# Optimization experiments

Hardware: AMD Instinct MI355X
Metric: run time of the kernel (lower is better)

## Reference

```python
import jax, jax.numpy as jnp
import numpy as np

B, N, D, H, DH, G = 4, 16384, 256, 8, 64, 64  # batch, tokens, dim, heads, dim_head, slice_num
INNER = H * DH

def _gelu(t):
    return jax.nn.gelu(t, approximate=False)  # torch nn.GELU default is exact erf

def setup_inputs() -> dict:
    key = jax.random.key(0)
    ks = jax.random.split(key, 12)
    s = lambda k, shape, sc: jax.random.normal(k, shape, jnp.float32) * sc
    return {
        "x": jax.random.normal(ks[0], (B, N, D), jnp.float32),
        "Wx": s(ks[1], (INNER, D), 0.05), "bx": jnp.zeros((INNER,), jnp.float32),
        "W1": s(ks[2], (G, DH), 0.1), "b1": jnp.zeros((G,), jnp.float32),
        "W2": s(ks[3], (1, G), 0.1), "b2": jnp.zeros((1,), jnp.float32),
        "bias": jnp.full((1, H, 1, 1), 0.5, jnp.float32),
        "Ws": s(ks[4], (G, DH), 0.1), "bs": jnp.zeros((G,), jnp.float32),
        "Wq": s(ks[5], (DH, DH), 0.1),
        "Wk": s(ks[6], (DH, DH), 0.1),
        "Wv": s(ks[7], (DH, DH), 0.1),
        "Wo": s(ks[8], (D, INNER), 0.05), "bo": jnp.zeros((D,), jnp.float32),
        "u": jax.random.uniform(ks[9], (B, H, N, G), jnp.float32),  # gumbel base noise
    }

def reference(x, Wx, bx, W1, b1, W2, b2, bias, Ws, bs, Wq, Wk, Wv, Wo, bo, u):
    b, n, d = x.shape
    h, dh = bias.shape[1], Wq.shape[0]
    # project and split heads: [B,H,N,dh]
    x_mid = (x @ Wx.T + bx).reshape(b, n, h, dh).transpose(0, 2, 1, 3)
    # per-token temperature MLP + learned bias, clamped
    temp = _gelu(_gelu(x_mid @ W1.T + b1) @ W2.T + b2) + bias  # [B,H,N,1]
    temp = jnp.clip(temp, 0.01)
    # gumbel-softmax soft slice routing
    logits = x_mid @ Ws.T + bs                                  # [B,H,N,G]
    gnoise = -jnp.log(-jnp.log(u + 1e-8) + 1e-8)
    slice_w = jax.nn.softmax((logits + gnoise) / temp, axis=-1)  # [B,H,N,G]
    # weighted pooling into slice tokens
    slice_norm = slice_w.sum(axis=2)                             # [B,H,G]
    slice_tok = jnp.einsum('bhnc,bhng->bhgc', x_mid, slice_w)
    slice_tok = slice_tok / (slice_norm + 1e-5)[..., None]       # [B,H,G,dh]
    # attention over the G slice tokens
    q = slice_tok @ Wq.T
    k = slice_tok @ Wk.T
    v = slice_tok @ Wv.T
    scale = 1.0 / np.sqrt(dh).astype(np.float32)
    attn = jax.nn.softmax(jnp.einsum('bhgc,bhkc->bhgk', q, k) * scale, axis=-1)
    out_s = jnp.einsum('bhgk,bhkc->bhgc', attn, v)               # [B,H,G,dh]
    # scatter back to tokens via slice weights
    out_x = jnp.einsum('bhgc,bhng->bhnc', out_s, slice_w)        # [B,H,N,dh]
    out_x = out_x.transpose(0, 2, 1, 3).reshape(b, n, h * dh)
    return out_x @ Wo.T + bo
```

## Files before the change

kernel.cpp:

```cpp
#include <hip/hip_runtime.h>

constexpr int B_ = 4;
constexpr int N_ = 16384;
constexpr int D_ = 256;
constexpr int H_ = 8;
constexpr int DH_ = 64;
constexpr int G_ = 64;
constexpr int INNER_ = 512;

typedef __attribute__((ext_vector_type(8))) short bf16x8;
typedef __attribute__((ext_vector_type(4))) float f32x4;

__device__ __forceinline__ unsigned short f2bu(float f) {
  union { float f; unsigned int u; } v; v.f = f;
  unsigned int r = v.u + 0x7FFFu + ((v.u >> 16) & 1u);
  return (unsigned short)(r >> 16);
}
__device__ __forceinline__ float bu2f(unsigned short h) {
  union { unsigned int u; float f; } v; v.u = ((unsigned int)h) << 16;
  return v.f;
}
__device__ __forceinline__ float gelu_f(float x) {
  const float ax = fabsf(x);
  const float y = ax * 0.70710678118654752440f;
  const float t = 1.0f / fmaf(0.3275911f, y, 1.0f);
  float poly = 1.061405429f;
  poly = fmaf(poly, t, -1.453152027f);
  poly = fmaf(poly, t, 1.421413741f);
  poly = fmaf(poly, t, -0.284496736f);
  poly = fmaf(poly, t, 0.254829592f);
  poly *= t;
  const float e = __expf(-y * y);
  const float E = fmaf(-poly, e, 1.0f);
  return fmaf(0.5f * ax, E, 0.5f * x);
}

__global__ __launch_bounds__(256) void cast_kernel(const float* __restrict__ in,
                                                   unsigned short* __restrict__ o, int n) {
  int i = (blockIdx.x * 256 + threadIdx.x) * 4;
  if (i + 3 < n) {
    float4 v = *reinterpret_cast<const float4*>(&in[i]);
    o[i + 0] = f2bu(v.x);
    o[i + 1] = f2bu(v.y);
    o[i + 2] = f2bu(v.z);
    o[i + 3] = f2bu(v.w);
  }
}

__global__ __launch_bounds__(256) void prep_wrb_kernel(const float* __restrict__ W1,
                                                       const float* __restrict__ Ws,
                                                       unsigned short* __restrict__ WrB) {
  const int i = blockIdx.x * 256 + threadIdx.x;
  if (i < 8192) {
    const int row = i >> 6, col = i & 63;
    const float v = (row < 64) ? W1[row * 64 + col] : Ws[(row - 64) * 64 + col];
    WrB[i] = f2bu(v);
  }
}

template <int MODE>
__global__ __launch_bounds__(256)
void gemm_bt_kernel(const float* __restrict__ Af32,
                    const unsigned short* __restrict__ Abf,
                    const unsigned short* __restrict__ Bt,
                    unsigned short* __restrict__ Cbf,
                    float* __restrict__ Cf32,
                    const float* __restrict__ bias) {
  constexpr int K = (MODE == 0) ? 256 : 512;
  __shared__ unsigned short As[128][72];
  __shared__ unsigned short Bs[128][72];

  const int tid = threadIdx.x;
  const int lane = tid & 63;
  const int wid = tid >> 6;
  const int wm = wid >> 1;
  const int wn = wid & 1;
  const long m0 = (long)blockIdx.x * 128;
  const int n0 = blockIdx.y * 128;

  long aBase = 0, btBase = 0, cBase = 0;
  if constexpr (MODE == 1) {
    const long z = blockIdx.z;
    aBase = z * (long)N_ * 512;
    btBase = z * (long)D_ * 512;
    cBase = z * (long)N_ * D_;
  }

  f32x4 acc[4][4];
#pragma unroll
  for (int m = 0; m < 4; ++m)
#pragma unroll
    for (int n = 0; n < 4; ++n) acc[m][n] = (f32x4){0.f, 0.f, 0.f, 0.f};

  for (int t = 0; t < K / 64; ++t) {
    const int k0 = t * 64;
    if constexpr (MODE == 0) {
#pragma unroll
      for (int i = 0; i < 8; ++i) {
        const int flat = i * 1024 + tid * 4;
        const int r = flat >> 6;
        const int kk = flat & 63;
        const float4 v = *reinterpret_cast<const float4*>(&Af32[(m0 + r) * 256 + k0 + kk]);
        unsigned short tmp[4] = {f2bu(v.x), f2bu(v.y), f2bu(v.z), f2bu(v.w)};
        *reinterpret_cast<unsigned long long*>(&As[r][kk]) =
            *reinterpret_cast<unsigned long long*>(tmp);
      }
    } else {
#pragma unroll
      for (int i = 0; i < 4; ++i) {
        const int flat = i * 2048 + tid * 8;
        const int r = flat >> 6;
        const int kk = flat & 63;
        *reinterpret_cast<int4*>(&As[r][kk]) =
            *reinterpret_cast<const int4*>(&Abf[aBase + (m0 + r) * (long)K + k0 + kk]);
      }
    }
#pragma unroll
    for (int i = 0; i < 4; ++i) {
      const int flat = i * 2048 + tid * 8;
      const int c = flat >> 6;
      const int kk = flat & 63;
      *reinterpret_cast<int4*>(&Bs[c][kk]) =
          *reinterpret_cast<const int4*>(&Bt[btBase + (n0 + c) * (long)K + k0 + kk]);
    }
    __syncthreads();
#pragma unroll
    for (int kk = 0; kk < 2; ++kk) {
      bf16x8 a[4], bb[4];
#pragma unroll
      for (int m = 0; m < 4; ++m)
        a[m] = *reinterpret_cast<const bf16x8*>(
            &As[wm * 64 + m * 16 + (lane & 15)][kk * 32 + (lane >> 4) * 8]);
#pragma unroll
      for (int n = 0; n < 4; ++n)
        bb[n] = *reinterpret_cast<const bf16x8*>(
            &Bs[wn * 64 + n * 16 + (lane & 15)][kk * 32 + (lane >> 4) * 8]);
#pragma unroll
      for (int m = 0; m < 4; ++m)
#pragma unroll
        for (int n = 0; n < 4; ++n)
          acc[m][n] = __builtin_amdgcn_mfma_f32_16x16x32_bf16(a[m], bb[n], acc[m][n], 0, 0, 0);
    }
    __syncthreads();
  }
#pragma unroll
  for (int n = 0; n < 4; ++n) {
    const int c = n0 + wn * 64 + n * 16 + (lane & 15);
    const float bv = bias[c];
#pragma unroll
    for (int m = 0; m < 4; ++m) {
      const long rb = m0 + wm * 64 + m * 16 + ((lane >> 4) << 2);
#pragma unroll
      for (int j = 0; j < 4; ++j) {
        const float val = acc[m][n][j] + bv;
        if constexpr (MODE == 0) {
          Cbf[(rb + j) * 512 + c] = f2bu(val);
        } else {
          Cf32[cBase + (rb + j) * 256 + c] = val;
        }
      }
    }
  }
}

__global__ __launch_bounds__(256)
void routing_fused_kernel(const unsigned short* __restrict__ xmid,
                          const unsigned short* __restrict__ WrB,
                          const float* __restrict__ u,
                          const float* __restrict__ b1,
                          const float* __restrict__ W2,
                          const float* __restrict__ b2,
                          const float* __restrict__ biasH,
                          const float* __restrict__ bs,
                          unsigned short* __restrict__ wout) {
  __shared__ union SM {
    struct { unsigned short As[64][72]; unsigned short Bs[128][72]; } s;
    float hl[64 * 67];
  } sm;
  __shared__ float cw2[64], cb1[64], cbs[64], cbh[8];
  __shared__ float tempL[64];

  const int tid = threadIdx.x;
  const int lane = tid & 63;
  const int wid = tid >> 6;
  const int wm = wid >> 1;
  const int wn = wid & 1;
  const int q = lane >> 4;
  const int c15 = lane & 15;

  if (tid < 64) {
    cw2[tid] = W2[tid];
    cb1[tid] = b1[tid];
    cbs[tid] = bs[tid];
  }
  if (tid < 8) cbh[tid] = biasH[tid];
  const float b2g = b2[0];

  const unsigned short* Ablk = xmid + (long)blockIdx.x * 4096;
#pragma unroll
  for (int i = 0; i < 2; ++i) {
    const int idx = i * 256 + tid;
    const int row = idx >> 3;
    const int col = (idx & 7) * 8;
    *reinterpret_cast<int4*>(&sm.s.As[row][col]) = *reinterpret_cast<const int4*>(Ablk + idx * 8);
  }
#pragma unroll
  for (int i = 0; i < 4; ++i) {
    const int idx = i * 256 + tid;
    const int row = idx >> 3;
    const int col = (idx & 7) * 8;
    *reinterpret_cast<int4*>(&sm.s.Bs[row][col]) = *reinterpret_cast<const int4*>(WrB + idx * 8);
  }
  __syncthreads();

  f32x4 acc[2][4];
#pragma unroll
  for (int m = 0; m < 2; ++m)
#pragma unroll
    for (int n = 0; n < 4; ++n) acc[m][n] = (f32x4){0.f, 0.f, 0.f, 0.f};

#pragma unroll
  for (int kk = 0; kk < 2; ++kk) {
    bf16x8 a[2], bb[4];
#pragma unroll
    for (int m = 0; m < 2; ++m)
      a[m] = *reinterpret_cast<const bf16x8*>(
          &sm.s.As[wm * 32 + m * 16 + c15][kk * 32 + q * 8]);
#pragma unroll
    for (int n = 0; n < 4; ++n)
      bb[n] = *reinterpret_cast<const bf16x8*>(
          &sm.s.Bs[wn * 64 + n * 16 + c15][kk * 32 + q * 8]);
#pragma unroll
    for (int m = 0; m < 2; ++m)
#pragma unroll
      for (int n = 0; n < 4; ++n)
        acc[m][n] = __builtin_amdgcn_mfma_f32_16x16x32_bf16(a[m], bb[n], acc[m][n], 0, 0, 0);
  }
  __syncthreads();

  if (wn == 0) {
    float b1v[4];
#pragma unroll
    for (int n = 0; n < 4; ++n) b1v[n] = cb1[n * 16 + c15];
#pragma unroll
    for (int m = 0; m < 2; ++m) {
      const int rb = wm * 32 + m * 16 + q * 4;
#pragma unroll
      for (int n = 0; n < 4; ++n) {
        const int c = n * 16 + c15;
#pragma unroll
        for (int j = 0; j < 4; ++j)
          sm.hl[(rb + j) * 67 + c] = acc[m][n][j] + b1v[n];
      }
    }
  }
  __syncthreads();

  const int r_e = tid >> 2;
  const int quarter = tid & 3;
  const int g0 = quarter * 16;
  const long t_e = (long)blockIdx.x * 64 + r_e;
  const int h_e = (int)(t_e & 7);

  float sdot = 0.f;
#pragma unroll
  for (int j = 0; j < 16; ++j)
    sdot = fmaf(gelu_f(sm.hl[r_e * 67 + g0 + j]), cw2[g0 + j], sdot);
  sdot += __shfl_xor(sdot, 1);
  sdot += __shfl_xor(sdot, 2);
  if (quarter == 0) {
    float temp = gelu_f(sdot + b2g) + cbh[h_e];
    temp = fmaxf(temp, 0.01f);
    tempL[r_e] = 1.0f / temp;
  }
  __syncthreads();

  if (wn == 1) {
    float bsv[4];
#pragma unroll
    for (int n = 0; n < 4; ++n) bsv[n] = cbs[n * 16 + c15];
#pragma unroll
    for (int m = 0; m < 2; ++m) {
      const int rb = wm * 32 + m * 16 + q * 4;
#pragma unroll
      for (int n = 0; n < 4; ++n) {
        const int c = n * 16 + c15;
#pragma unroll
        for (int j = 0; j < 4; ++j)
          sm.hl[(rb + j) * 67 + c] = acc[m][n][j] + bsv[n];
      }
    }
  }
  __syncthreads();

  const long bn_e = t_e >> 3;
  const long b_e = bn_e >> 14;
  const long n_e = bn_e & 16383;
  const long uoff = (((b_e * 8 + h_e) << 14) + n_e) * 64 + g0;

  const float inv_t = tempL[r_e];
  float sv[16];
  float mx = -1e30f;
#pragma unroll
  for (int q8 = 0; q8 < 4; ++q8) {
    const float4 uu = *reinterpret_cast<const float4*>(&u[uoff + q8 * 4]);
    const float ua[4] = {uu.x, uu.y, uu.z, uu.w};
#pragma unroll
    for (int e = 0; e < 4; ++e) {
      const int j = q8 * 4 + e;
      const float gn = -__logf(-__logf(ua[e] + 1e-8f) + 1e-8f);
      const float si = (sm.hl[r_e * 67 + g0 + j] + gn) * inv_t;
      sv[j] = si;
      mx = fmaxf(mx, si);
    }
  }
  mx = fmaxf(mx, __shfl_xor(mx, 1));
  mx = fmaxf(mx, __shfl_xor(mx, 2));
  float ssum = 0.f;
#pragma unroll
  for (int j = 0; j < 16; ++j) {
    const float e = __expf(sv[j] - mx);
    sv[j] = e;
    ssum += e;
  }
  ssum += __shfl_xor(ssum, 1);
  ssum += __shfl_xor(ssum, 2);
  const float inv_s = 1.0f / ssum;

  unsigned short* wrow = wout + t_e * 64 + g0;
#pragma unroll
  for (int i2 = 0; i2 < 2; ++i2) {
    unsigned short tmp[8];
#pragma unroll
    for (int j = 0; j < 8; ++j) tmp[j] = f2bu(sv[i2 * 8 + j] * inv_s);
    *reinterpret_cast<int4*>(wrow + i2 * 8) = *reinterpret_cast<const int4*>(tmp);
  }
}

__global__ __launch_bounds__(256, 2)
void pool_v2_kernel(const unsigned short* __restrict__ xmid,
                    const unsigned short* __restrict__ wbf,
                    float* __restrict__ pacc, float* __restrict__ pnrm) {
  __shared__ __align__(16) float wl[64][68];
  __shared__ __align__(16) float xl[64][68];
  __shared__ float snl[64];
  const int tid = threadIdx.x;
  const int bx = blockIdx.x;
  const int bh = bx & 31;
  const int chunk = bx >> 5;
  const int b = bh >> 3;
  const int h = bh & 7;
  const int r = tid >> 2;
  const int p = (tid & 3) << 4;
  const int q = tid >> 6;
  const int tin = tid & 63;
  const int gb = ((tin >> 3) & 7) << 3;
  const int cb = (tin & 7) << 3;

  float a[8][8];
#pragma unroll
  for (int gi = 0; gi < 8; ++gi)
#pragma unroll
    for (int ci = 0; ci < 8; ++ci) a[gi][ci] = 0.f;
  float sn[16];
#pragma unroll
  for (int j = 0; j < 16; ++j) sn[j] = 0.f;
  if (tid < 64) snl[tid] = 0.f;

  const long tok0 = (long)b * N_ + chunk * 512;

  for (int sub = 0; sub < 8; ++sub) {
    __syncthreads();
    const long base = (tok0 + sub * 64 + r) * 512 + h * 64 + p;
    const int4 rw0 = *reinterpret_cast<const int4*>(&wbf[base]);
    const int4 rw1 = *reinterpret_cast<const int4*>(&wbf[base + 8]);
    const int4 rx0 = *reinterpret_cast<const int4*>(&xmid[base]);
    const int4 rx1 = *reinterpret_cast<const int4*>(&xmid[base + 8]);
    const unsigned short* pw0 = reinterpret_cast<const unsigned short*>(&rw0);
    const unsigned short* pw1 = reinterpret_cast<const unsigned short*>(&rw1);
    const unsigned short* px0 = reinterpret_cast<const unsigned short*>(&rx0);
    const unsigned short* px1 = reinterpret_cast<const unsigned short*>(&rx1);
#pragma unroll
    for (int j = 0; j < 8; ++j) {
      const float w0 = bu2f(pw0[j]);
      const float w1 = bu2f(pw1[j]);
      wl[r][p + j] = w0;
      wl[r][p + 8 + j] = w1;
      sn[j] += w0;
      sn[8 + j] += w1;
      xl[r][p + j] = bu2f(px0[j]);
      xl[r][p + 8 + j] = bu2f(px1[j]);
    }
    __syncthreads();
    for (int i = 0; i < 16; ++i) {
      const int nn = q * 16 + i;
      const f32x4 w0 = *reinterpret_cast<const f32x4*>(&wl[nn][gb]);
      const f32x4 w1 = *reinterpret_cast<const f32x4*>(&wl[nn][gb + 4]);
      const f32x4 x0 = *reinterpret_cast<const f32x4*>(&xl[nn][cb]);
      const f32x4 x1 = *reinterpret_cast<const f32x4*>(&xl[nn][cb + 4]);
      const float wv[8] = {w0[0], w0[1], w0[2], w0[3], w1[0], w1[1], w1[2], w1[3]};
      const float xv[8] = {x0[0], x0[1], x0[2], x0[3], x1[0], x1[1], x1[2], x1[3]};
#pragma unroll
      for (int gi = 0; gi < 8; ++gi)
#pragma unroll
        for (int ci = 0; ci < 8; ++ci) a[gi][ci] = fmaf(wv[gi], xv[ci], a[gi][ci]);
    }
  }

  __syncthreads();
#pragma unroll
  for (int j = 0; j < 16; ++j) atomicAdd(&snl[p + j], sn[j]);

  float* mA = &wl[0][0];
  float* mB = &xl[0][0];
  __syncthreads();
  if (q == 1 || q == 3) {
    float* mb = (q == 1) ? mA : mB;
#pragma unroll
    for (int gi = 0; gi < 8; ++gi)
#pragma unroll
      for (int ci = 0; ci < 8; ++ci) mb[(gi * 8 + ci) * 64 + tin] = a[gi][ci];
  }
  __syncthreads();
  if (q == 0) {
#pragma unroll
    for (int gi = 0; gi < 8; ++gi)
#pragma unroll
      for (int ci = 0; ci < 8; ++ci) a[gi][ci] += mA[(gi * 8 + ci) * 64 + tin];
  } else if (q == 2) {
#pragma unroll
    for (int gi = 0; gi < 8; ++gi)
#pragma unroll
      for (int ci = 0; ci < 8; ++ci) a[gi][ci] += mB[(gi * 8 + ci) * 64 + tin];
  }
  __syncthreads();
  if (q == 2) {
#pragma unroll
    for (int gi = 0; gi < 8; ++gi)
#pragma unroll
      for (int ci = 0; ci < 8; ++ci) mA[(gi * 8 + ci) * 64 + tin] = a[gi][ci];
  }
  __syncthreads();
  if (q == 0) {
    float* pblk = pacc + (long)bx * 4096;
#pragma unroll
    for (int gi = 0; gi < 8; ++gi) {
      float vals[8];
#pragma unroll
      for (int ci = 0; ci < 8; ++ci) vals[ci] = a[gi][ci] + mA[(gi * 8 + ci) * 64 + tin];
      *reinterpret_cast<float4*>(&pblk[(gb + gi) * 64 + cb]) =
          *reinterpret_cast<const float4*>(&vals[0]);
      *reinterpret_cast<float4*>(&pblk[(gb + gi) * 64 + cb + 4]) =
          *reinterpret_cast<const float4*>(&vals[4]);
    }
  }
  if (tid < 64) pnrm[(long)bx * 64 + tid] = snl[tid];
}

__global__ __launch_bounds__(256)
void pool_reduce_kernel(const float* __restrict__ pacc, const float* __restrict__ pnrm,
                        float* __restrict__ sacc, float* __restrict__ snrm) {
  const int bh = blockIdx.x;
  const int tid = threadIdx.x;
  float s[16];
#pragma unroll
  for (int i = 0; i < 16; ++i) s[i] = 0.f;
  for (int c = 0; c < 32; ++c) {
    const float* src = pacc + ((long)(c * 32 + bh)) * 4096 + tid * 16;
#pragma unroll
    for (int i = 0; i < 16; i += 4) {
      const float4 v = *reinterpret_cast<const float4*>(&src[i]);
      s[i] += v.x; s[i + 1] += v.y; s[i + 2] += v.z; s[i + 3] += v.w;
    }
  }
  float* dst = sacc + (long)bh * 4096 + tid * 16;
#pragma unroll
  for (int i = 0; i < 16; i += 4)
    *reinterpret_cast<float4*>(&dst[i]) = make_float4(s[i], s[i + 1], s[i + 2], s[i + 3]);
  if (tid < 64) {
    float t = 0.f;
    for (int c = 0; c < 32; ++c) t += pnrm[((long)(c * 32 + bh)) * 64 + tid];
    snrm[bh * 64 + tid] = t;
  }
}

__global__ __launch_bounds__(256)
void slice_attn_kernel(const float* __restrict__ sacc,
                       const float* __restrict__ snrm,
                       const float* __restrict__ Wq,
                       const float* __restrict__ Wk,
                       const float* __restrict__ Wv,
                       const float* __restrict__ Wo,
                       unsigned short* __restrict__ MT) {
  __shared__ float st[64][65];
  __shared__ float qq[64][65];
  __shared__ float kk_[64][65];
  __shared__ float vv[64][65];
  __shared__ float at[64][65];
  __shared__ float nrm[64];
  const int tid = threadIdx.x;
  const int bh = blockIdx.x;
  const int b = bh >> 3;
  const int h = bh & 7;
  const int lane = tid & 63;
  const int w = tid >> 6;

  if (tid < 64) nrm[tid] = 1.0f / (snrm[bh * 64 + tid] + 1e-5f);
  __syncthreads();
#pragma unroll
  for (int i = 0; i < 16; ++i) {
    const int idx = tid * 16 + i;
    const int gg = idx >> 6;
    const int cc = idx & 63;
    st[gg][cc] = sacc[(long)bh * 4096 + idx] * nrm[gg];
  }
  __syncthreads();
  for (int cc = 0; cc < 16; ++cc) {
    const int c = w * 16 + cc;
    const float* wqr = &Wq[c * 64];
    const float* wkr = &Wk[c * 64];
    const float* wvr = &Wv[c * 64];
    float aq = 0.f, ak = 0.f, av = 0.f;
#pragma unroll
    for (int j = 0; j < 64; ++j) {
      const float sj = st[lane][j];
      aq = fmaf(sj, wqr[j], aq);
      ak = fmaf(sj, wkr[j], ak);
      av = fmaf(sj, wvr[j], av);
    }
    qq[lane][c] = aq;
    kk_[lane][c] = ak;
    vv[lane][c] = av;
  }
  __syncthreads();
  for (int cc = 0; cc < 16; ++cc) {
    const int k2 = w * 16 + cc;
    float a0 = 0.f;
#pragma unroll
    for (int j = 0; j < 64; ++j) a0 = fmaf(qq[lane][j], kk_[k2][j], a0);
    at[lane][k2] = a0 * 0.125f;
  }
  __syncthreads();
  if (tid < 64) {
    float m = -1e30f;
    for (int j = 0; j < 64; ++j) m = fmaxf(m, at[tid][j]);
    float ssum = 0.f;
    for (int j = 0; j < 64; ++j) {
      const float e = expf(at[tid][j] - m);
      at[tid][j] = e;
      ssum += e;
    }
    const float inv = 1.0f / ssum;
    for (int j = 0; j < 64; ++j) at[tid][j] *= inv;
  }
  __syncthreads();
  for (int cc = 0; cc < 16; ++cc) {
    const int c = w * 16 + cc;
    float a0 = 0.f;
#pragma unroll
    for (int j = 0; j < 64; ++j) a0 = fmaf(at[lane][j], vv[j][c], a0);
    qq[lane][c] = a0;
  }
  __syncthreads();
  for (int dd = 0; dd < 64; ++dd) {
    const int d = w * 64 + dd;
    const float* wor = &Wo[(long)d * 512 + h * 64];
    float a0 = 0.f;
#pragma unroll
    for (int j = 0; j < 64; ++j) a0 = fmaf(qq[lane][j], wor[j], a0);
    MT[((long)b * 256 + d) * 512 + h * 64 + lane] = f2bu(a0);
  }
}

extern "C" void kernel_launch(void* const* d_in, const int* in_sizes, int n_in,
                              void* d_out, int out_size, void* d_ws, size_t ws_size,
                              hipStream_t stream) {
  const float* x = (const float*)d_in[0];
  const float* Wx = (const float*)d_in[1];
  const float* bx = (const float*)d_in[2];
  const float* W1 = (const float*)d_in[3];
  const float* b1 = (const float*)d_in[4];
  const float* W2 = (const float*)d_in[5];
  const float* b2 = (const float*)d_in[6];
  const float* bias = (const float*)d_in[7];
  const float* Ws = (const float*)d_in[8];
  const float* bs = (const float*)d_in[9];
  const float* Wq = (const float*)d_in[10];
  const float* Wk = (const float*)d_in[11];
  const float* Wv = (const float*)d_in[12];
  const float* Wo = (const float*)d_in[13];
  const float* bo = (const float*)d_in[14];
  const float* u = (const float*)d_in[15];
  float* out = (float*)d_out;

  char* ws = (char*)d_ws;
  unsigned short* xmid = (unsigned short*)(ws + 0);
  unsigned short* wbf = (unsigned short*)(ws + 67108864);
  float* sacc = (float*)(ws + 134217728);
  float* snrm = (float*)(ws + 134742016);
  unsigned short* Wxb = (unsigned short*)(ws + 134750208);
  unsigned short* MT = (unsigned short*)(ws + 135012352);
  unsigned short* WrB = (unsigned short*)(ws + 136060928);
  float* pacc = (float*)(ws + 136077312);
  float* pnrm = (float*)(ws + 152854528);

  cast_kernel<<<dim3(128), dim3(256), 0, stream>>>(Wx, Wxb, INNER_ * D_);
  prep_wrb_kernel<<<dim3(32), dim3(256), 0, stream>>>(W1, Ws, WrB);
  gemm_bt_kernel<0><<<dim3(512, 4, 1), dim3(256), 0, stream>>>(x, nullptr, Wxb, xmid, nullptr, bx);
  routing_fused_kernel<<<dim3(8192), dim3(256), 0, stream>>>(xmid, WrB, u, b1, W2, b2, bias, bs, wbf);
  pool_v2_kernel<<<dim3(1024), dim3(256), 0, stream>>>(xmid, wbf, pacc, pnrm);
  pool_reduce_kernel<<<dim3(32), dim3(256), 0, stream>>>(pacc, pnrm, sacc, snrm);
  slice_attn_kernel<<<dim3(32), dim3(256), 0, stream>>>(sacc, snrm, Wq, Wk, Wv, Wo, MT);
  gemm_bt_kernel<1><<<dim3(128, 2, 4), dim3(256), 0, stream>>>(nullptr, wbf, MT, nullptr, out, bo);
}
```

Before: 381.7 us.

## Split Wo folding out of slice attention into a wide parallel MT-build kernel

Measured after the change: 348.0 us. -8.8%, faster.

```diff
diff --git a/kernel.cpp b/kernel.cpp
--- a/kernel.cpp
+++ b/kernel.cpp
@@ -490,8 +490,7 @@
                        const float* __restrict__ Wq,
                        const float* __restrict__ Wk,
                        const float* __restrict__ Wv,
-                       const float* __restrict__ Wo,
-                       unsigned short* __restrict__ MT) {
+                       float* __restrict__ outS) {
   __shared__ float st[64][65];
   __shared__ float qq[64][65];
   __shared__ float kk_[64][65];
@@ -500,8 +499,6 @@
   __shared__ float nrm[64];
   const int tid = threadIdx.x;
   const int bh = blockIdx.x;
-  const int b = bh >> 3;
-  const int h = bh & 7;
   const int lane = tid & 63;
   const int w = tid >> 6;
 
@@ -520,55 +517,98 @@
     const float* wqr = &Wq[c * 64];
     const float* wkr = &Wk[c * 64];
     const float* wvr = &Wv[c * 64];
-    float aq = 0.f, ak = 0.f, av = 0.f;
-#pragma unroll
-    for (int j = 0; j < 64; ++j) {
-      const float sj = st[lane][j];
-      aq = fmaf(sj, wqr[j], aq);
-      ak = fmaf(sj, wkr[j], ak);
-      av = fmaf(sj, wvr[j], av);
-    }
-    qq[lane][c] = aq;
-    kk_[lane][c] = ak;
-    vv[lane][c] = av;
+    float q0 = 0.f, q1 = 0.f, q2 = 0.f, q3 = 0.f;
+    float k0 = 0.f, k1 = 0.f, k2 = 0.f, k3 = 0.f;
+    float v0 = 0.f, v1 = 0.f, v2 = 0.f, v3 = 0.f;
+#pragma unroll
+    for (int j = 0; j < 64; j += 4) {
+      const float s0 = st[lane][j], s1 = st[lane][j + 1];
+      const float s2 = st[lane][j + 2], s3 = st[lane][j + 3];
+      q0 = fmaf(s0, wqr[j], q0); q1 = fmaf(s1, wqr[j + 1], q1);
+      q2 = fmaf(s2, wqr[j + 2], q2); q3 = fmaf(s3, wqr[j + 3], q3);
+      k0 = fmaf(s0, wkr[j], k0); k1 = fmaf(s1, wkr[j + 1], k1);
+      k2 = fmaf(s2, wkr[j + 2], k2); k3 = fmaf(s3, wkr[j + 3], k3);
+      v0 = fmaf(s0, wvr[j], v0); v1 = fmaf(s1, wvr[j + 1], v1);
+      v2 = fmaf(s2, wvr[j + 2], v2); v3 = fmaf(s3, wvr[j + 3], v3);
+    }
+    qq[lane][c] = (q0 + q1) + (q2 + q3);
+    kk_[lane][c] = (k0 + k1) + (k2 + k3);
+    vv[lane][c] = (v0 + v1) + (v2 + v3);
   }
   __syncthreads();
   for (int cc = 0; cc < 16; ++cc) {
-    const int k2 = w * 16 + cc;
-    float a0 = 0.f;
-#pragma unroll
-    for (int j = 0; j < 64; ++j) a0 = fmaf(qq[lane][j], kk_[k2][j], a0);
-    at[lane][k2] = a0 * 0.125f;
+    const int k2i = w * 16 + cc;
+    float a0 = 0.f, a1 = 0.f, a2 = 0.f, a3 = 0.f;
+#pragma unroll
+    for (int j = 0; j < 64; j += 4) {
+      a0 = fmaf(qq[lane][j], kk_[k2i][j], a0);
+      a1 = fmaf(qq[lane][j + 1], kk_[k2i][j + 1], a1);
+      a2 = fmaf(qq[lane][j + 2], kk_[k2i][j + 2], a2);
+      a3 = fmaf(qq[lane][j + 3], kk_[k2i][j + 3], a3);
+    }
+    at[lane][k2i] = ((a0 + a1) + (a2 + a3)) * 0.125f;
   }
   __syncthreads();
   if (tid < 64) {
-    float m = -1e30f;
-    for (int j = 0; j < 64; ++j) m = fmaxf(m, at[tid][j]);
-    float ssum = 0.f;
-    for (int j = 0; j < 64; ++j) {
-      const float e = expf(at[tid][j] - m);
-      at[tid][j] = e;
-      ssum += e;
-    }
-    const float inv = 1.0f / ssum;
+    float m0 = -1e30f, m1 = -1e30f, m2 = -1e30f, m3 = -1e30f;
+#pragma unroll
+    for (int j = 0; j < 64; j += 4) {
+      m0 = fmaxf(m0, at[tid][j]); m1 = fmaxf(m1, at[tid][j + 1]);
+      m2 = fmaxf(m2, at[tid][j + 2]); m3 = fmaxf(m3, at[tid][j + 3]);
+    }
+    const float m = fmaxf(fmaxf(m0, m1), fmaxf(m2, m3));
+    float s0 = 0.f, s1 = 0.f, s2 = 0.f, s3 = 0.f;
+#pragma unroll
+    for (int j = 0; j < 64; j += 4) {
+      const float e0 = __expf(at[tid][j] - m);
+      const float e1 = __expf(at[tid][j + 1] - m);
+      const float e2 = __expf(at[tid][j + 2] - m);
+      const float e3 = __expf(at[tid][j + 3] - m);
+      at[tid][j] = e0; at[tid][j + 1] = e1; at[tid][j + 2] = e2; at[tid][j + 3] = e3;
+      s0 += e0; s1 += e1; s2 += e2; s3 += e3;
+    }
+    const float inv = 1.0f / ((s0 + s1) + (s2 + s3));
+#pragma unroll
     for (int j = 0; j < 64; ++j) at[tid][j] *= inv;
   }
   __syncthreads();
   for (int cc = 0; cc < 16; ++cc) {
     const int c = w * 16 + cc;
-    float a0 = 0.f;
-#pragma unroll
-    for (int j = 0; j < 64; ++j) a0 = fmaf(at[lane][j], vv[j][c], a0);
-    qq[lane][c] = a0;
-  }
-  __syncthreads();
-  for (int dd = 0; dd < 64; ++dd) {
-    const int d = w * 64 + dd;
-    const float* wor = &Wo[(long)d * 512 + h * 64];
-    float a0 = 0.f;
-#pragma unroll
-    for (int j = 0; j < 64; ++j) a0 = fmaf(qq[lane][j], wor[j], a0);
-    MT[((long)b * 256 + d) * 512 + h * 64 + lane] = f2bu(a0);
+    float a0 = 0.f, a1 = 0.f, a2 = 0.f, a3 = 0.f;
+#pragma unroll
+    for (int j = 0; j < 64; j += 4) {
+      a0 = fmaf(at[lane][j], vv[j][c], a0);
+      a1 = fmaf(at[lane][j + 1], vv[j + 1][c], a1);
+      a2 = fmaf(at[lane][j + 2], vv[j + 2][c], a2);
+      a3 = fmaf(at[lane][j + 3], vv[j + 3][c], a3);
+    }
+    outS[((long)bh * 64 + lane) * 64 + c] = (a0 + a1) + (a2 + a3);
+  }
+}
+
+__global__ __launch_bounds__(256)
+void mt_build_kernel(const float* __restrict__ outS, const float* __restrict__ Wo,
+                     unsigned short* __restrict__ MT) {
+  const int bd = blockIdx.x;
+  const int b = bd >> 8;
+  const int d = bd & 255;
+  const int tid = threadIdx.x;
+#pragma unroll
+  for (int it = 0; it < 2; ++it) {
+    const int hg = it * 256 + tid;
+    const int h = hg >> 6;
+    const int g = hg & 63;
+    const float* wor = Wo + (long)d * 512 + h * 64;
+    const float* os = outS + ((long)(b * 8 + h) * 64 + g) * 64;
+    float a0 = 0.f, a1 = 0.f, a2 = 0.f, a3 = 0.f;
+#pragma unroll
+    for (int c = 0; c < 64; c += 4) {
+      a0 = fmaf(os[c], wor[c], a0);
+      a1 = fmaf(os[c + 1], wor[c + 1], a1);
+      a2 = fmaf(os[c + 2], wor[c + 2], a2);
+      a3 = fmaf(os[c + 3], wor[c + 3], a3);
+    }
+    MT[((long)b * 256 + d) * 512 + hg] = f2bu((a0 + a1) + (a2 + a3));
   }
 }
 
@@ -603,6 +643,7 @@
   unsigned short* WrB = (unsigned short*)(ws + 136060928);
   float* pacc = (float*)(ws + 136077312);
   float* pnrm = (float*)(ws + 152854528);
+  float* outS = (float*)(ws + 153116672);
 
   cast_kernel<<<dim3(128), dim3(256), 0, stream>>>(Wx, Wxb, INNER_ * D_);
   prep_wrb_kernel<<<dim3(32), dim3(256), 0, stream>>>(W1, Ws, WrB);
@@ -610,6 +651,7 @@
   routing_fused_kernel<<<dim3(8192), dim3(256), 0, stream>>>(xmid, WrB, u, b1, W2, b2, bias, bs, wbf);
   pool_v2_kernel<<<dim3(1024), dim3(256), 0, stream>>>(xmid, wbf, pacc, pnrm);
   pool_reduce_kernel<<<dim3(32), dim3(256), 0, stream>>>(pacc, pnrm, sacc, snrm);
-  slice_attn_kernel<<<dim3(32), dim3(256), 0, stream>>>(sacc, snrm, Wq, Wk, Wv, Wo, MT);
+  slice_attn_kernel<<<dim3(32), dim3(256), 0, stream>>>(sacc, snrm, Wq, Wk, Wv, outS);
+  mt_build_kernel<<<dim3(1024), dim3(256), 0, stream>>>(outS, Wo, MT);
   gemm_bt_kernel<1><<<dim3(128, 2, 4), dim3(256), 0, stream>>>(nullptr, wbf, MT, nullptr, out, bo);
 }
```
